# Performance work log

Measured on AMD Instinct MI355X. Metric: run time of the kernel, lower is better.

## Reference

```python
import jax, jax.numpy as jnp
import numpy as np

B, N, S = 256, 512, 32
D_ENT, D_KEY, D_IN, D_FUNC, D_TYPE, H = 256, 32, 1024, 256, 259, 32


def _init_linear(k, out_d, in_d):
    kw, kb = jax.random.split(k)
    bound = 1.0 / np.sqrt(in_d)
    W = jax.random.uniform(kw, (out_d, in_d), minval=-bound, maxval=bound, dtype=jnp.float32)
    b = jax.random.uniform(kb, (out_d,), minval=-bound, maxval=bound, dtype=jnp.float32)
    return W, b


def setup_inputs() -> dict:
    key = jax.random.key(0)
    ks = jax.random.split(key, 16)
    inp = {
        "embedding": jax.random.normal(ks[0], (B, D_IN), jnp.float32),
        "available_unit_type_mask": (jax.random.uniform(ks[1], (B, D_TYPE)) < 0.5).astype(jnp.float32),
        "available_units_mask": jnp.ones((B, N), jnp.float32),
        "entity_embedding": jax.random.normal(ks[2], (B, N, D_ENT), jnp.float32),
        "selected_units": jax.random.randint(ks[3], (B, S), 0, N, dtype=jnp.int32),
        "end_embedding": jax.random.uniform(ks[4], (1, D_KEY), minval=-1.0, maxval=1.0, dtype=jnp.float32) / np.sqrt(D_KEY),
    }
    inp["W_key"], inp["b_key"] = _init_linear(ks[5], D_KEY, D_ENT)
    inp["W_func"], inp["b_func"] = _init_linear(ks[6], D_FUNC, D_TYPE)
    inp["W_fc1"], inp["b_fc1"] = _init_linear(ks[7], D_FUNC, D_IN)
    inp["W_fc2"], inp["b_fc2"] = _init_linear(ks[8], D_KEY, D_FUNC)
    inp["W_embed"], inp["b_embed"] = _init_linear(ks[9], D_IN, D_KEY)
    inp["W_ih"], inp["b_ih"] = _init_linear(ks[10], 4 * H, D_KEY)
    inp["W_hh"], inp["b_hh"] = _init_linear(ks[11], 4 * H, H)
    return inp


def reference(embedding, available_unit_type_mask, available_units_mask, entity_embedding,
              selected_units, end_embedding, W_key, b_key, W_func, b_func, W_fc1, b_fc1,
              W_fc2, b_fc2, W_embed, b_embed, W_ih, b_ih, W_hh, b_hh):
    Bv, Nv, _ = entity_embedding.shape
    Sv = selected_units.shape[1]
    # keys for each entity + end-flag embedding appended -> [B, N+1, key_dim]
    key_t = jnp.einsum('bnd,kd->bnk', entity_embedding, W_key) + b_key
    end = jnp.broadcast_to(end_embedding[None, :, :], (Bv, 1, end_embedding.shape[1]))
    pad_key = jnp.concatenate([key_t, end], axis=1)
    # mask: entities + end flag; teacher-forced selected positions forced to 1
    mask0 = jnp.concatenate([available_units_mask, jnp.ones((Bv, 1), available_units_mask.dtype)], axis=1)
    mask0 = mask0.at[jnp.arange(Bv)[:, None], selected_units].set(1.0)
    func_embed = jax.nn.relu(available_unit_type_mask @ W_func.T + b_func)
    inv_n = 1.0 / jnp.float32(Nv)  # split_entity_num = end_flag_index = num_units
    bidx = jnp.arange(Bv)
    # per-step selected index (dummy 0 on the final end-flag step) and validity
    sel_seq = jnp.concatenate([selected_units.T, jnp.zeros((1, Bv), selected_units.dtype)], axis=0)
    valid_seq = jnp.concatenate([jnp.ones((Sv, Bv), jnp.float32), jnp.zeros((1, Bv), jnp.float32)], axis=0)

    def step(carry, xs):
        emb, h, c, mask = carry
        sel, valid = xs
        # query = fc2(relu(fc1(emb) + func_embed))
        x = jax.nn.relu(emb @ W_fc1.T + b_fc1 + func_embed) @ W_fc2.T + b_fc2
        # one LSTM step
        gates = x @ W_ih.T + b_ih + h @ W_hh.T + b_hh
        i_g, f_g, g_g, o_g = jnp.split(gates, 4, axis=1)
        c = jax.nn.sigmoid(f_g) * c + jax.nn.sigmoid(i_g) * jnp.tanh(g_g)
        h = jax.nn.sigmoid(o_g) * jnp.tanh(c)
        # masked dot-product over keys -> logits [B, N+1]
        q = jnp.einsum('bk,bnk->bn', h, pad_key) - (1.0 - mask) * 1e9
        # mark selected unit unavailable for subsequent steps
        mask = mask.at[bidx, sel].set(jnp.where(valid > 0, 0.0, mask[bidx, sel]))
        # one-hot gather of selected key, averaged, fed back into embedding
        emb_sel = pad_key[bidx, sel] * inv_n
        emb = emb + (emb_sel @ W_embed.T + b_embed) * valid[:, None]
        return (emb, h, c, mask), q

    h0 = jnp.zeros((Bv, W_hh.shape[1]), jnp.float32)
    c0 = jnp.zeros_like(h0)
    (emb, _, _, _), logits = jax.lax.scan(step, (embedding, h0, c0, mask0), (sel_seq, valid_seq))
    logits = jnp.transpose(logits, (1, 0, 2))  # [B, S+1, N+1]
    return logits, emb
```

## Files before the change

### kernel.cpp

```cpp
#include <hip/hip_runtime.h>
#include <math.h>

#define BB_ 256
#define NN_ 512
#define SS_ 32
#define NP1 513
#define SP1 33
#define D_IN 1024
#define D_TYPE 259
#define INV_N (1.0f/512.0f)

#define N_ACT 256
#define COMB_BASE 256
#define END_BID 258
#define KEY_BASE 259
#define N_KEY 2048
#define FRONT_GRID (KEY_BASE + N_KEY)

typedef short s16x4 __attribute__((ext_vector_type(4)));
typedef short s16x8 __attribute__((ext_vector_type(8)));
typedef float f32x4 __attribute__((ext_vector_type(4)));

#if defined(__has_builtin)
#if __has_builtin(__builtin_amdgcn_rcpf)
#define FRCP(x) __builtin_amdgcn_rcpf(x)
#else
#define FRCP(x) (1.0f / (x))
#endif
#else
#define FRCP(x) (1.0f / (x))
#endif

__device__ __forceinline__ float fsig(float x) { return FRCP(1.0f + __expf(-x)); }
__device__ __forceinline__ float ftanh(float x) { return fmaf(-2.0f, FRCP(1.0f + __expf(2.0f * x)), 1.0f); }
__device__ __forceinline__ short f2bf(float f) {
    unsigned u = __float_as_uint(f);
    unsigned r = (u + 0x7FFFu + ((u >> 16) & 1u)) >> 16;
    return (short)r;
}
__device__ __forceinline__ float bf2f(short s) {
    unsigned u = ((unsigned)(unsigned short)s) << 16;
    return __uint_as_float(u);
}

__global__ __launch_bounds__(256) void front_kernel(
    const float* __restrict__ ent, const float* __restrict__ Wk,
    const float* __restrict__ bk, const float* __restrict__ endv,
    const float* __restrict__ Wemb, const float* __restrict__ bemb,
    const float* __restrict__ Wfc1, const float* __restrict__ emb0,
    const float* __restrict__ bfc1, const float* __restrict__ atm,
    const float* __restrict__ Wf, const float* __restrict__ bf,
    short* __restrict__ pkbf, float* __restrict__ WcombT,
    float* __restrict__ cbv, float* __restrict__ act_pre)
{
    __shared__ __align__(128) char u_raw[33280];
    short* a_st   = (short*)u_raw;
    float* wemb_s = (float*)(u_raw + 18688);
    float* a_lds  = (float*)u_raw;
    float* w_lds  = (float*)(u_raw + 16640);

    const int tid = threadIdx.x;
    const int bid = blockIdx.x;
    const int lane = tid & 63, w = tid >> 6;
    const int nl = lane & 15, q = lane >> 4;

    if (bid >= KEY_BASE) {
        const size_t rowbase = (size_t)(bid - KEY_BASE) * 64;
        const int rl = w * 16 + nl;
        const float* arow = ent + ((rowbase + (size_t)rl) << 8) + q * 8;

        float4 aR[16];
#pragma unroll
        for (int kk = 0; kk < 8; kk++) {
            aR[kk * 2]     = *(const float4*)(arow + kk * 32);
            aR[kk * 2 + 1] = *(const float4*)(arow + kk * 32 + 4);
        }

        const float* brow0 = Wk + (size_t)nl * 256 + q * 8;
        const float* brow1 = Wk + (size_t)(16 + nl) * 256 + q * 8;

        f32x4 acc0 = (f32x4)0.0f, acc1 = (f32x4)0.0f;
#pragma unroll
        for (int kk = 0; kk < 8; kk++) {
            float4 b00 = *(const float4*)(brow0 + kk * 32);
            float4 b01 = *(const float4*)(brow0 + kk * 32 + 4);
            float4 b10 = *(const float4*)(brow1 + kk * 32);
            float4 b11 = *(const float4*)(brow1 + kk * 32 + 4);
            s16x8 af, bf0, bf1;
            float4 a0 = aR[kk * 2], a1 = aR[kk * 2 + 1];
            af[0] = f2bf(a0.x); af[1] = f2bf(a0.y); af[2] = f2bf(a0.z); af[3] = f2bf(a0.w);
            af[4] = f2bf(a1.x); af[5] = f2bf(a1.y); af[6] = f2bf(a1.z); af[7] = f2bf(a1.w);
            bf0[0] = f2bf(b00.x); bf0[1] = f2bf(b00.y); bf0[2] = f2bf(b00.z); bf0[3] = f2bf(b00.w);
            bf0[4] = f2bf(b01.x); bf0[5] = f2bf(b01.y); bf0[6] = f2bf(b01.z); bf0[7] = f2bf(b01.w);
            bf1[0] = f2bf(b10.x); bf1[1] = f2bf(b10.y); bf1[2] = f2bf(b10.z); bf1[3] = f2bf(b10.w);
            bf1[4] = f2bf(b11.x); bf1[5] = f2bf(b11.y); bf1[6] = f2bf(b11.z); bf1[7] = f2bf(b11.w);
            acc0 = __builtin_amdgcn_mfma_f32_16x16x32_bf16(af, bf0, acc0, 0, 0, 0);
            acc1 = __builtin_amdgcn_mfma_f32_16x16x32_bf16(af, bf1, acc1, 0, 0, 0);
        }

        float bkv0 = bk[nl], bkv1 = bk[16 + nl];
#pragma unroll
        for (int r = 0; r < 4; r++) {
            int rowg = (int)rowbase + w * 16 + q * 4 + r;
            int b = rowg >> 9, n = rowg & 511;
            pkbf[((size_t)b * NP1 + n) * 32 + nl]      = f2bf(acc0[r] + bkv0);
            pkbf[((size_t)b * NP1 + n) * 32 + 16 + nl] = f2bf(acc1[r] + bkv1);
        }
    } else if (bid < N_ACT) {
        const int idx = bid;
        const int jt = idx & 15, bt = idx >> 4;
        const int bb = tid >> 4, jj = tid & 15;

#pragma unroll 4
        for (int r = 0; r < 16; r++) {
            a_lds[r * 260 + tid] = atm[(size_t)(bt * 16 + r) * D_TYPE + tid];
            w_lds[r * 260 + tid] = Wf[(size_t)(jt * 16 + r) * D_TYPE + tid];
            if (tid < 3) {
                a_lds[r * 260 + 256 + tid] = atm[(size_t)(bt * 16 + r) * D_TYPE + 256 + tid];
                w_lds[r * 260 + 256 + tid] = Wf[(size_t)(jt * 16 + r) * D_TYPE + 256 + tid];
            }
        }
        __syncthreads();
        float accf;
        {
            float f0 = 0.0f, f1 = 0.0f, f2 = 0.0f, f3 = 0.0f;
            const float4* ap = (const float4*)&a_lds[bb * 260];
            const float4* wp = (const float4*)&w_lds[jj * 260];
#pragma unroll 8
            for (int i4 = 0; i4 < 64; i4++) {
                float4 a = ap[i4]; float4 wv = wp[i4];
                f0 = fmaf(a.x, wv.x, f0); f1 = fmaf(a.y, wv.y, f1);
                f2 = fmaf(a.z, wv.z, f2); f3 = fmaf(a.w, wv.w, f3);
            }
            accf = (f0 + f1) + (f2 + f3);
            for (int i = 256; i < 259; i++) accf = fmaf(a_lds[bb * 260 + i], w_lds[jj * 260 + i], accf);
        }
        float c0 = 0.0f, c1 = 0.0f, c2 = 0.0f, c3 = 0.0f;
        for (int c = 0; c < 4; c++) {
            __syncthreads();
#pragma unroll
            for (int p = 0; p < 4; p++) {
                int l4 = p * 256 + tid;
                int r = l4 >> 6, k4 = l4 & 63;
                *(float4*)&a_lds[r * 260 + k4 * 4] =
                    *(const float4*)(emb0 + (size_t)(bt * 16 + r) * D_IN + c * 256 + k4 * 4);
                *(float4*)&w_lds[r * 260 + k4 * 4] =
                    *(const float4*)(Wfc1 + (size_t)(jt * 16 + r) * D_IN + c * 256 + k4 * 4);
            }
            __syncthreads();
#pragma unroll 8
            for (int k4 = 0; k4 < 64; k4++) {
                float4 a = *(const float4*)&a_lds[bb * 260 + k4 * 4];
                float4 wv = *(const float4*)&w_lds[jj * 260 + k4 * 4];
                c0 = fmaf(a.x, wv.x, c0); c1 = fmaf(a.y, wv.y, c1);
                c2 = fmaf(a.z, wv.z, c2); c3 = fmaf(a.w, wv.w, c3);
            }
        }
        float acc = (c0 + c1) + (c2 + c3);
        const int b = bt * 16 + bb, j = jt * 16 + jj;
        act_pre[b * 256 + j] = acc + bfc1[j] + fmaxf(accf + bf[j], 0.0f);
    } else if (bid < END_BID) {
        const int m0 = bid - COMB_BASE;
        f32x4 acc[2][3];
#pragma unroll
        for (int mt = 0; mt < 2; mt++)
#pragma unroll
            for (int t = 0; t < 3; t++) acc[mt][t] = (f32x4)0.0f;

        for (int kc = 0; kc < 16; ++kc) {
            __syncthreads();
#pragma unroll
            for (int p = 0; p < 8; p++) {
                int flat = p * 256 + tid;
                int row = flat >> 4;
                int f4 = flat & 15;
                float4 v = *(const float4*)(Wfc1 + (size_t)(m0 * 128 + row) * D_IN + kc * 64 + f4 * 4);
                s16x4 sv;
                sv[0] = f2bf(v.x); sv[1] = f2bf(v.y); sv[2] = f2bf(v.z); sv[3] = f2bf(v.w);
                *(s16x4*)&a_st[row * 72 + f4 * 4] = sv;
            }
            {
                int r = tid >> 2, c0 = tid & 3;
#pragma unroll
                for (int cc = 0; cc < 9; cc++) {
                    int col = c0 + cc * 4;
                    if (col < 33) {
                        float v = (col < 32) ? Wemb[(size_t)(kc * 64 + r) * 32 + col]
                                             : bemb[kc * 64 + r];
                        wemb_s[r * 33 + col] = v;
                    }
                }
            }
            __syncthreads();
#pragma unroll
            for (int ks = 0; ks < 2; ks++) {
                s16x8 bv[3];
#pragma unroll
                for (int t = 0; t < 3; t++) {
                    int n = t * 16 + nl;
#pragma unroll
                    for (int jj = 0; jj < 8; jj++) {
                        float v = (n < 33) ? wemb_s[(ks * 32 + q * 8 + jj) * 33 + n] : 0.0f;
                        bv[t][jj] = f2bf(v);
                    }
                }
#pragma unroll
                for (int mt = 0; mt < 2; mt++) {
                    s16x8 af = *(const s16x8*)&a_st[(w * 32 + mt * 16 + nl) * 72 + ks * 32 + q * 8];
#pragma unroll
                    for (int t = 0; t < 3; t++)
                        acc[mt][t] = __builtin_amdgcn_mfma_f32_16x16x32_bf16(af, bv[t], acc[mt][t], 0, 0, 0);
                }
            }
        }
#pragma unroll
        for (int mt = 0; mt < 2; mt++)
#pragma unroll
            for (int t = 0; t < 3; t++)
#pragma unroll
                for (int r = 0; r < 4; r++) {
                    int j = m0 * 128 + w * 32 + mt * 16 + q * 4 + r;
                    int n = t * 16 + nl;
                    if (n < 32) WcombT[j * 32 + n] = acc[mt][t][r];
                    else if (n == 32) cbv[j] = acc[mt][t][r];
                }
    } else {
        const int k = tid & 31, b0 = tid >> 5;
        short evk = f2bf(endv[k]);
        for (int b = b0; b < BB_; b += 8)
            pkbf[((size_t)b * NP1 + 512) * 32 + k] = evk;
    }
}

__global__ __launch_bounds__(256, 1) void back_kernel(
    const short* __restrict__ pkbf, const float* __restrict__ act_pre0,
    const int* __restrict__ sel, const float* __restrict__ avail,
    const float* __restrict__ Wfc2, const float* __restrict__ bfc2,
    const float* __restrict__ Wih, const float* __restrict__ bih,
    const float* __restrict__ bhh, const float* __restrict__ Whh,
    const float* __restrict__ WcombT, const float* __restrict__ cbv,
    const float* __restrict__ emb0, const float* __restrict__ Wemb,
    const float* __restrict__ bemb,
    float* __restrict__ logits, float* __restrict__ emb_out)
{
    __shared__ float S[19204];
    __shared__ int sel_l[SS_];
    float* rap_l  = S;
    float* red_l  = S + 8580;
    float* x_l    = S + 17028;
    float* cumE_l = S + 18084;
    float* ssel_l = S + 19140;
    float* xg_l   = S;
    float* h_all  = S + 4224;
    float* m0_l   = S + 8580;
    int*   tf_l   = (int*)(S + 9093);

    const int tid = threadIdx.x;
    const int b = blockIdx.x;
    const int lane = tid & 63, w = tid >> 6;
    const int nl = lane & 15, q = lane >> 4;

    if (tid < SS_) sel_l[tid] = sel[b * SS_ + tid];

    {
        const int k = tid & 31, sq = tid >> 5;
        const int sq4 = sq * 4;
        int s0 = sel[b * SS_ + sq4 + 0];
        int s1 = sel[b * SS_ + sq4 + 1];
        int s2 = sel[b * SS_ + sq4 + 2];
        int s3 = sel[b * SS_ + sq4 + 3];
        float v0 = bf2f(pkbf[((size_t)b * NP1 + s0) * 32 + k]) * INV_N;
        float v1 = bf2f(pkbf[((size_t)b * NP1 + s1) * 32 + k]) * INV_N;
        float v2 = bf2f(pkbf[((size_t)b * NP1 + s2) * 32 + k]) * INV_N;
        float v3 = bf2f(pkbf[((size_t)b * NP1 + s3) * 32 + k]) * INV_N;
        float p0 = v0, p1 = p0 + v1, p2 = p1 + v2, p3 = p2 + v3;
        x_l[sq * 32 + k] = p3;
        __syncthreads();
        float off = 0.0f;
        for (int p = 0; p < 8; p++) if (p < sq) off += x_l[p * 32 + k];
        cumE_l[(sq4 + 1) * 32 + k] = off + p0;
        cumE_l[(sq4 + 2) * 32 + k] = off + p1;
        cumE_l[(sq4 + 3) * 32 + k] = off + p2;
        cumE_l[(sq4 + 4) * 32 + k] = off + p3;
        if (tid < 32) cumE_l[tid] = 0.0f;
        if (sq == 7) ssel_l[k] = off + p3;
    }
    __syncthreads();

    {
        float wcr[32];
#pragma unroll
        for (int k4 = 0; k4 < 8; k4++) {
            float4 v = *(const float4*)(WcombT + (size_t)tid * 32 + k4 * 4);
            wcr[k4*4] = v.x; wcr[k4*4+1] = v.y; wcr[k4*4+2] = v.z; wcr[k4*4+3] = v.w;
        }
        const float cbr = cbv[tid];
        const float ap0v = act_pre0[b * 256 + tid];
        for (int t = 0; t < SP1; ++t) {
            float ap = fmaf((float)t, cbr, ap0v);
            const float4* ce = (const float4*)&cumE_l[t * 32];
#pragma unroll
            for (int k4 = 0; k4 < 8; k4++) {
                float4 e = ce[k4];
                ap = fmaf(e.x, wcr[k4*4], ap);   ap = fmaf(e.y, wcr[k4*4+1], ap);
                ap = fmaf(e.z, wcr[k4*4+2], ap); ap = fmaf(e.w, wcr[k4*4+3], ap);
            }
            rap_l[t * 260 + tid] = fmaxf(ap, 0.0f);
        }
    }
    __syncthreads();

    {
        const int seg = tid >> 5, i = tid & 31;
        float wfc2r[32];
#pragma unroll
        for (int i4 = 0; i4 < 8; i4++) {
            float4 v = *(const float4*)(Wfc2 + (size_t)i * 256 + seg * 32 + i4 * 4);
            wfc2r[i4*4] = v.x; wfc2r[i4*4+1] = v.y; wfc2r[i4*4+2] = v.z; wfc2r[i4*4+3] = v.w;
        }
        for (int t = 0; t < SP1; ++t) {
            float part = 0.0f;
            const float4* rp = (const float4*)&rap_l[t * 260 + seg * 32];
#pragma unroll
            for (int i4 = 0; i4 < 8; i4++) {
                float4 rv = rp[i4];
                part = fmaf(rv.x, wfc2r[i4*4], part);   part = fmaf(rv.y, wfc2r[i4*4+1], part);
                part = fmaf(rv.z, wfc2r[i4*4+2], part); part = fmaf(rv.w, wfc2r[i4*4+3], part);
            }
            red_l[t * 256 + seg * 32 + i] = part;
        }
    }
    __syncthreads();

    for (int p = 0; p < 5; p++) {
        int idx = p * 256 + tid;
        if (idx < SP1 * 32) {
            int t = idx >> 5, i = idx & 31;
            float x = bfc2[i];
#pragma unroll
            for (int s = 0; s < 8; s++) x += red_l[t * 256 + s * 32 + i];
            x_l[t * 32 + i] = x;
        }
    }
    __syncthreads();

    {
        const int g = tid & 127, half = tid >> 7;
        float wihr[32];
#pragma unroll
        for (int k4 = 0; k4 < 8; k4++) {
            float4 v = *(const float4*)(Wih + (size_t)g * 32 + k4 * 4);
            wihr[k4*4] = v.x; wihr[k4*4+1] = v.y; wihr[k4*4+2] = v.z; wihr[k4*4+3] = v.w;
        }
        const float bihg = bih[g] + bhh[g];
        for (int t = half; t < SP1; t += 2) {
            float gg = bihg;
            const float4* xp = (const float4*)&x_l[t * 32];
#pragma unroll
            for (int k4 = 0; k4 < 8; k4++) {
                float4 xv = xp[k4];
                gg = fmaf(xv.x, wihr[k4*4], gg);   gg = fmaf(xv.y, wihr[k4*4+1], gg);
                gg = fmaf(xv.z, wihr[k4*4+2], gg); gg = fmaf(xv.w, wihr[k4*4+3], gg);
            }
            xg_l[t * 128 + g] = gg;
        }
    }
    __syncthreads();

    if (tid < 64) {
        float whh0[32], whh1[32];
#pragma unroll
        for (int k4 = 0; k4 < 8; k4++) {
            float4 v0 = *(const float4*)(Whh + (size_t)tid * 32 + k4 * 4);
            float4 v1 = *(const float4*)(Whh + (size_t)(tid + 64) * 32 + k4 * 4);
            whh0[k4*4] = v0.x; whh0[k4*4+1] = v0.y; whh0[k4*4+2] = v0.z; whh0[k4*4+3] = v0.w;
            whh1[k4*4] = v1.x; whh1[k4*4+1] = v1.y; whh1[k4*4+2] = v1.z; whh1[k4*4+3] = v1.w;
        }
        float c = 0.0f, h = 0.0f;
        for (int t = 0; t < SP1; ++t) {
            float g0 = xg_l[t * 128 + tid];
            float g1 = xg_l[t * 128 + 64 + tid];
            if (t > 0) {
#pragma unroll
                for (int k = 0; k < 32; k++) {
                    float hk = __shfl(h, k);
                    g0 = fmaf(hk, whh0[k], g0);
                    g1 = fmaf(hk, whh1[k], g1);
                }
            }
            float og0 = __shfl_xor(g0, 32);
            float og1 = __shfl_xor(g1, 32);
            float ig = fsig(g0);
            float fg = fsig(og0);
            float gv = ftanh(g1);
            float og = fsig(og1);
            float cn = fg * c + ig * gv;
            float hn = og * ftanh(cn);
            if (tid < 32) {
                c = cn; h = hn;
                h_all[t * 32 + tid] = hn;
            }
        }
    } else {
        for (int n = tid - 64; n < NP1; n += 192) {
            float m = (n < NN_) ? avail[(size_t)b * NN_ + n] : 1.0f;
            int tf = 1000;
#pragma unroll 8
            for (int s = 0; s < SS_; s++) {
                int sv = sel_l[s];
                if (sv == n) { m = 1.0f; if (s < tf) tf = s; }
            }
            m0_l[n] = m; tf_l[n] = tf;
        }
    }
    __syncthreads();

    {
        s16x8 afr[3];
#pragma unroll
        for (int mt = 0; mt < 3; mt++) {
            int row = mt * 16 + nl;
            s16x8 av;
#pragma unroll
            for (int jj = 0; jj < 8; jj++) {
                float v = (row < SP1) ? h_all[row * 32 + q * 8 + jj] : 0.0f;
                av[jj] = f2bf(v);
            }
            afr[mt] = av;
        }
        for (int tt = w; tt < 33; tt += 4) {
            int n = tt * 16 + nl;
            bool nv = n < NP1;
            s16x8 bv = nv ? *(const s16x8*)(pkbf + ((size_t)b * NP1 + n) * 32 + q * 8) : (s16x8)0;
            f32x4 acc[3];
#pragma unroll
            for (int mt = 0; mt < 3; mt++)
                acc[mt] = __builtin_amdgcn_mfma_f32_16x16x32_bf16(afr[mt], bv, (f32x4)0.0f, 0, 0, 0);
            float m0v = nv ? m0_l[n] : 0.0f;
            int tfv = nv ? tf_l[n] : 0;
#pragma unroll
            for (int mt = 0; mt < 3; mt++)
#pragma unroll
                for (int r = 0; r < 4; r++) {
                    int t = mt * 16 + q * 4 + r;
                    if (t < SP1 && nv) {
                        float mv = (t <= tfv) ? m0v : 0.0f;
                        logits[((size_t)b * SP1 + t) * NP1 + n] = acc[mt][r] - (1.0f - mv) * 1e9f;
                    }
                }
        }
    }

#pragma unroll
    for (int p = 0; p < 4; p++) {
        int i = p * 256 + tid;
        float acc = emb0[(size_t)b * D_IN + i] + 32.0f * bemb[i];
        const float* wr = Wemb + (size_t)i * 32;
#pragma unroll
        for (int k4 = 0; k4 < 8; k4++) {
            float4 wv = *(const float4*)(wr + k4 * 4);
            acc = fmaf(ssel_l[k4*4+0], wv.x, acc);
            acc = fmaf(ssel_l[k4*4+1], wv.y, acc);
            acc = fmaf(ssel_l[k4*4+2], wv.z, acc);
            acc = fmaf(ssel_l[k4*4+3], wv.w, acc);
        }
        emb_out[(size_t)b * D_IN + i] = acc;
    }
}

extern "C" void kernel_launch(void* const* d_in, const int* in_sizes, int n_in,
                              void* d_out, int out_size, void* d_ws, size_t ws_size,
                              hipStream_t stream)
{
    (void)in_sizes; (void)n_in; (void)out_size; (void)ws_size;
    const float* embedding = (const float*)d_in[0];
    const float* atm       = (const float*)d_in[1];
    const float* avail     = (const float*)d_in[2];
    const float* ent       = (const float*)d_in[3];
    const int*   sel       = (const int*)  d_in[4];
    const float* endv      = (const float*)d_in[5];
    const float* Wk   = (const float*)d_in[6];
    const float* bk   = (const float*)d_in[7];
    const float* Wf   = (const float*)d_in[8];
    const float* bf   = (const float*)d_in[9];
    const float* Wfc1 = (const float*)d_in[10];
    const float* bfc1 = (const float*)d_in[11];
    const float* Wfc2 = (const float*)d_in[12];
    const float* bfc2 = (const float*)d_in[13];
    const float* Wemb = (const float*)d_in[14];
    const float* bemb = (const float*)d_in[15];
    const float* Wih  = (const float*)d_in[16];
    const float* bih  = (const float*)d_in[17];
    const float* Whh  = (const float*)d_in[18];
    const float* bhh  = (const float*)d_in[19];

    float* ws = (float*)d_ws;
    float* act_pre = ws;
    float* WcombT  = act_pre + BB_ * 256;
    float* cbv     = WcombT + 256 * 32;
    short* pkbf    = (short*)(cbv + 256);

    float* logits  = (float*)d_out;
    float* emb_out = logits + (size_t)BB_ * SP1 * NP1;

    front_kernel<<<FRONT_GRID, 256, 0, stream>>>(ent, Wk, bk, endv, Wemb, bemb,
                                                 Wfc1, embedding, bfc1, atm, Wf, bf,
                                                 pkbf, WcombT, cbv, act_pre);
    back_kernel<<<BB_, 256, 0, stream>>>(pkbf, act_pre, sel, avail,
                                         Wfc2, bfc2, Wih, bih, bhh, Whh,
                                         WcombT, cbv, embedding, Wemb, bemb,
                                         logits, emb_out);
}
```

Baseline: 334.6 us.

## Split key projection into separate kernel with LDS-staged bf16 weights

Moves the entity-key projection out of the combined front kernel into its own kernel. Each block converts W_key to bf16 once into swizzled shared memory instead of having every thread reload and reconvert it from global memory. Entity-row loads are double-buffered to lower register pressure, and occupancy is raised through launch bounds. The cost is one extra kernel launch and a dependency boundary between the key and misc work, which previously ran in the same grid.

```diff
diff --git a/kernel.cpp b/kernel.cpp
--- a/kernel.cpp
+++ b/kernel.cpp
@@ -13,9 +13,8 @@
 #define N_ACT 256
 #define COMB_BASE 256
 #define END_BID 258
-#define KEY_BASE 259
+#define MISC_GRID 259
 #define N_KEY 2048
-#define FRONT_GRID (KEY_BASE + N_KEY)
 
 typedef short s16x4 __attribute__((ext_vector_type(4)));
 typedef short s16x8 __attribute__((ext_vector_type(8)));
@@ -43,9 +42,75 @@
     return __uint_as_float(u);
 }
 
-__global__ __launch_bounds__(256) void front_kernel(
+__global__ __launch_bounds__(256, 5) void keys_kernel(
     const float* __restrict__ ent, const float* __restrict__ Wk,
-    const float* __restrict__ bk, const float* __restrict__ endv,
+    const float* __restrict__ bk, short* __restrict__ pkbf)
+{
+    __shared__ short Bs[8192];
+
+    const int tid = threadIdx.x;
+    const int lane = tid & 63, w = tid >> 6;
+    const int nl = lane & 15, q = lane >> 4;
+
+#pragma unroll
+    for (int p = 0; p < 4; p++) {
+        int id = p * 256 + tid;
+        int n = id >> 5, cg = id & 31;
+        float4 v0 = *(const float4*)(Wk + (size_t)n * 256 + cg * 8);
+        float4 v1 = *(const float4*)(Wk + (size_t)n * 256 + cg * 8 + 4);
+        s16x8 sv;
+        sv[0] = f2bf(v0.x); sv[1] = f2bf(v0.y); sv[2] = f2bf(v0.z); sv[3] = f2bf(v0.w);
+        sv[4] = f2bf(v1.x); sv[5] = f2bf(v1.y); sv[6] = f2bf(v1.z); sv[7] = f2bf(v1.w);
+        int sw = (n & 7) << 1;
+        *(s16x8*)((char*)Bs + n * 512 + (((cg * 2) ^ sw) << 3)) = sv;
+    }
+    __syncthreads();
+
+    const int rl = w * 16 + nl;
+    const int swr = (nl & 7) << 1;
+#define BFRAG(t_, kk_) (*(const s16x8*)((const char*)Bs + \
+        (size_t)((t_) * 16 + nl) * 512 + ((((kk_) * 8 + q * 2) ^ swr) << 3)))
+
+    const size_t rowbase = (size_t)blockIdx.x * 64;
+    const float* arow = ent + ((rowbase + (size_t)rl) << 8) + q * 8;
+
+    float4 buf[4][2];
+#pragma unroll
+    for (int kk = 0; kk < 4; kk++) {
+        buf[kk][0] = *(const float4*)(arow + kk * 32);
+        buf[kk][1] = *(const float4*)(arow + kk * 32 + 4);
+    }
+
+    f32x4 acc0 = (f32x4)0.0f, acc1 = (f32x4)0.0f;
+#pragma unroll
+    for (int kk = 0; kk < 8; kk++) {
+        float4 a0 = buf[kk & 3][0], a1 = buf[kk & 3][1];
+        if (kk < 4) {
+            buf[kk & 3][0] = *(const float4*)(arow + (kk + 4) * 32);
+            buf[kk & 3][1] = *(const float4*)(arow + (kk + 4) * 32 + 4);
+        }
+        s16x8 af;
+        af[0] = f2bf(a0.x); af[1] = f2bf(a0.y); af[2] = f2bf(a0.z); af[3] = f2bf(a0.w);
+        af[4] = f2bf(a1.x); af[5] = f2bf(a1.y); af[6] = f2bf(a1.z); af[7] = f2bf(a1.w);
+        s16x8 b0 = BFRAG(0, kk);
+        s16x8 b1 = BFRAG(1, kk);
+        acc0 = __builtin_amdgcn_mfma_f32_16x16x32_bf16(af, b0, acc0, 0, 0, 0);
+        acc1 = __builtin_amdgcn_mfma_f32_16x16x32_bf16(af, b1, acc1, 0, 0, 0);
+    }
+#undef BFRAG
+
+    float bkv0 = bk[nl], bkv1 = bk[16 + nl];
+#pragma unroll
+    for (int r = 0; r < 4; r++) {
+        int rowg = (int)rowbase + w * 16 + q * 4 + r;
+        int b = rowg >> 9, n = rowg & 511;
+        pkbf[((size_t)b * NP1 + n) * 32 + nl]      = f2bf(acc0[r] + bkv0);
+        pkbf[((size_t)b * NP1 + n) * 32 + 16 + nl] = f2bf(acc1[r] + bkv1);
+    }
+}
+
+__global__ __launch_bounds__(256) void misc_kernel(
+    const float* __restrict__ endv,
     const float* __restrict__ Wemb, const float* __restrict__ bemb,
     const float* __restrict__ Wfc1, const float* __restrict__ emb0,
     const float* __restrict__ bfc1, const float* __restrict__ atm,
@@ -64,49 +129,7 @@
     const int lane = tid & 63, w = tid >> 6;
     const int nl = lane & 15, q = lane >> 4;
 
-    if (bid >= KEY_BASE) {
-        const size_t rowbase = (size_t)(bid - KEY_BASE) * 64;
-        const int rl = w * 16 + nl;
-        const float* arow = ent + ((rowbase + (size_t)rl) << 8) + q * 8;
-
-        float4 aR[16];
-#pragma unroll
-        for (int kk = 0; kk < 8; kk++) {
-            aR[kk * 2]     = *(const float4*)(arow + kk * 32);
-            aR[kk * 2 + 1] = *(const float4*)(arow + kk * 32 + 4);
-        }
-
-        const float* brow0 = Wk + (size_t)nl * 256 + q * 8;
-        const float* brow1 = Wk + (size_t)(16 + nl) * 256 + q * 8;
-
-        f32x4 acc0 = (f32x4)0.0f, acc1 = (f32x4)0.0f;
-#pragma unroll
-        for (int kk = 0; kk < 8; kk++) {
-            float4 b00 = *(const float4*)(brow0 + kk * 32);
-            float4 b01 = *(const float4*)(brow0 + kk * 32 + 4);
-            float4 b10 = *(const float4*)(brow1 + kk * 32);
-            float4 b11 = *(const float4*)(brow1 + kk * 32 + 4);
-            s16x8 af, bf0, bf1;
-            float4 a0 = aR[kk * 2], a1 = aR[kk * 2 + 1];
-            af[0] = f2bf(a0.x); af[1] = f2bf(a0.y); af[2] = f2bf(a0.z); af[3] = f2bf(a0.w);
-            af[4] = f2bf(a1.x); af[5] = f2bf(a1.y); af[6] = f2bf(a1.z); af[7] = f2bf(a1.w);
-            bf0[0] = f2bf(b00.x); bf0[1] = f2bf(b00.y); bf0[2] = f2bf(b00.z); bf0[3] = f2bf(b00.w);
-            bf0[4] = f2bf(b01.x); bf0[5] = f2bf(b01.y); bf0[6] = f2bf(b01.z); bf0[7] = f2bf(b01.w);
-            bf1[0] = f2bf(b10.x); bf1[1] = f2bf(b10.y); bf1[2] = f2bf(b10.z); bf1[3] = f2bf(b10.w);
-            bf1[4] = f2bf(b11.x); bf1[5] = f2bf(b11.y); bf1[6] = f2bf(b11.z); bf1[7] = f2bf(b11.w);
-            acc0 = __builtin_amdgcn_mfma_f32_16x16x32_bf16(af, bf0, acc0, 0, 0, 0);
-            acc1 = __builtin_amdgcn_mfma_f32_16x16x32_bf16(af, bf1, acc1, 0, 0, 0);
-        }
-
-        float bkv0 = bk[nl], bkv1 = bk[16 + nl];
-#pragma unroll
-        for (int r = 0; r < 4; r++) {
-            int rowg = (int)rowbase + w * 16 + q * 4 + r;
-            int b = rowg >> 9, n = rowg & 511;
-            pkbf[((size_t)b * NP1 + n) * 32 + nl]      = f2bf(acc0[r] + bkv0);
-            pkbf[((size_t)b * NP1 + n) * 32 + 16 + nl] = f2bf(acc1[r] + bkv1);
-        }
-    } else if (bid < N_ACT) {
+    if (bid < N_ACT) {
         const int idx = bid;
         const int jt = idx & 15, bt = idx >> 4;
         const int bb = tid >> 4, jj = tid & 15;
@@ -503,9 +526,10 @@
     float* logits  = (float*)d_out;
     float* emb_out = logits + (size_t)BB_ * SP1 * NP1;
 
-    front_kernel<<<FRONT_GRID, 256, 0, stream>>>(ent, Wk, bk, endv, Wemb, bemb,
-                                                 Wfc1, embedding, bfc1, atm, Wf, bf,
-                                                 pkbf, WcombT, cbv, act_pre);
+    keys_kernel<<<N_KEY, 256, 0, stream>>>(ent, Wk, bk, pkbf);
+    misc_kernel<<<MISC_GRID, 256, 0, stream>>>(endv, Wemb, bemb,
+                                               Wfc1, embedding, bfc1, atm, Wf, bf,
+                                               pkbf, WcombT, cbv, act_pre);
     back_kernel<<<BB_, 256, 0, stream>>>(pkbf, act_pre, sel, avail,
                                          Wfc2, bfc2, Wih, bih, bhh, Whh,
                                          WcombT, cbv, embedding, Wemb, bemb,
```

Measured after the change: 353.3 us. 1.06x slower.

## Split Wcomb reduction across blocks, hoist Wk fragments, reorder front grid

Applied to the files above, without the earlier changes.

The Wfc1·Wemb combination was computed by two blocks looping over 16 K-chunks. It is now split-K over 32 blocks that each handle one chunk and accumulate into zero-initialised outputs with atomicAdd, which removes a long serial tail from the front kernel. Key-projection blocks now come first in the grid, convert their Wk fragments to bf16 once before loading activations, and the kernel requests 4 blocks per CU through launch bounds. In exchange it adds a memset launch, float atomics that make the summation order nondeterministic, and more register pressure from the hoisted fragments.

```diff
diff --git a/kernel.cpp b/kernel.cpp
--- a/kernel.cpp
+++ b/kernel.cpp
@@ -10,12 +10,11 @@
 #define D_TYPE 259
 #define INV_N (1.0f/512.0f)
 
-#define N_ACT 256
-#define COMB_BASE 256
-#define END_BID 258
-#define KEY_BASE 259
 #define N_KEY 2048
-#define FRONT_GRID (KEY_BASE + N_KEY)
+#define ACT_BASE 2048
+#define COMB_BASE 2304
+#define END_BID 2336
+#define FRONT_GRID 2337
 
 typedef short s16x4 __attribute__((ext_vector_type(4)));
 typedef short s16x8 __attribute__((ext_vector_type(8)));
@@ -43,7 +42,7 @@
     return __uint_as_float(u);
 }
 
-__global__ __launch_bounds__(256) void front_kernel(
+__global__ __launch_bounds__(256, 4) void front_kernel(
     const float* __restrict__ ent, const float* __restrict__ Wk,
     const float* __restrict__ bk, const float* __restrict__ endv,
     const float* __restrict__ Wemb, const float* __restrict__ bemb,
@@ -64,38 +63,41 @@
     const int lane = tid & 63, w = tid >> 6;
     const int nl = lane & 15, q = lane >> 4;
 
-    if (bid >= KEY_BASE) {
-        const size_t rowbase = (size_t)(bid - KEY_BASE) * 64;
+    if (bid < N_KEY) {
+        const size_t rowbase = (size_t)bid * 64;
         const int rl = w * 16 + nl;
+
+        s16x8 bfr[8][2];
+#pragma unroll
+        for (int s = 0; s < 8; s++)
+#pragma unroll
+            for (int t = 0; t < 2; t++) {
+                const float* src = Wk + (size_t)(t * 16 + nl) * 256 + s * 32 + q * 8;
+                float4 v0 = *(const float4*)(src);
+                float4 v1 = *(const float4*)(src + 4);
+                s16x8 bv;
+                bv[0] = f2bf(v0.x); bv[1] = f2bf(v0.y); bv[2] = f2bf(v0.z); bv[3] = f2bf(v0.w);
+                bv[4] = f2bf(v1.x); bv[5] = f2bf(v1.y); bv[6] = f2bf(v1.z); bv[7] = f2bf(v1.w);
+                bfr[s][t] = bv;
+            }
+
         const float* arow = ent + ((rowbase + (size_t)rl) << 8) + q * 8;
-
         float4 aR[16];
 #pragma unroll
         for (int kk = 0; kk < 8; kk++) {
-            aR[kk * 2]     = *(const float4*)(arow + kk * 32);
-            aR[kk * 2 + 1] = *(const float4*)(arow + kk * 32 + 4);
-        }
-
-        const float* brow0 = Wk + (size_t)nl * 256 + q * 8;
-        const float* brow1 = Wk + (size_t)(16 + nl) * 256 + q * 8;
+            aR[2 * kk]     = *(const float4*)(arow + kk * 32);
+            aR[2 * kk + 1] = *(const float4*)(arow + kk * 32 + 4);
+        }
 
         f32x4 acc0 = (f32x4)0.0f, acc1 = (f32x4)0.0f;
 #pragma unroll
         for (int kk = 0; kk < 8; kk++) {
-            float4 b00 = *(const float4*)(brow0 + kk * 32);
-            float4 b01 = *(const float4*)(brow0 + kk * 32 + 4);
-            float4 b10 = *(const float4*)(brow1 + kk * 32);
-            float4 b11 = *(const float4*)(brow1 + kk * 32 + 4);
-            s16x8 af, bf0, bf1;
-            float4 a0 = aR[kk * 2], a1 = aR[kk * 2 + 1];
+            float4 a0 = aR[2 * kk], a1 = aR[2 * kk + 1];
+            s16x8 af;
             af[0] = f2bf(a0.x); af[1] = f2bf(a0.y); af[2] = f2bf(a0.z); af[3] = f2bf(a0.w);
             af[4] = f2bf(a1.x); af[5] = f2bf(a1.y); af[6] = f2bf(a1.z); af[7] = f2bf(a1.w);
-            bf0[0] = f2bf(b00.x); bf0[1] = f2bf(b00.y); bf0[2] = f2bf(b00.z); bf0[3] = f2bf(b00.w);
-            bf0[4] = f2bf(b01.x); bf0[5] = f2bf(b01.y); bf0[6] = f2bf(b01.z); bf0[7] = f2bf(b01.w);
-            bf1[0] = f2bf(b10.x); bf1[1] = f2bf(b10.y); bf1[2] = f2bf(b10.z); bf1[3] = f2bf(b10.w);
-            bf1[4] = f2bf(b11.x); bf1[5] = f2bf(b11.y); bf1[6] = f2bf(b11.z); bf1[7] = f2bf(b11.w);
-            acc0 = __builtin_amdgcn_mfma_f32_16x16x32_bf16(af, bf0, acc0, 0, 0, 0);
-            acc1 = __builtin_amdgcn_mfma_f32_16x16x32_bf16(af, bf1, acc1, 0, 0, 0);
+            acc0 = __builtin_amdgcn_mfma_f32_16x16x32_bf16(af, bfr[kk][0], acc0, 0, 0, 0);
+            acc1 = __builtin_amdgcn_mfma_f32_16x16x32_bf16(af, bfr[kk][1], acc1, 0, 0, 0);
         }
 
         float bkv0 = bk[nl], bkv1 = bk[16 + nl];
@@ -106,8 +108,8 @@
             pkbf[((size_t)b * NP1 + n) * 32 + nl]      = f2bf(acc0[r] + bkv0);
             pkbf[((size_t)b * NP1 + n) * 32 + 16 + nl] = f2bf(acc1[r] + bkv1);
         }
-    } else if (bid < N_ACT) {
-        const int idx = bid;
+    } else if (bid < COMB_BASE) {
+        const int idx = bid - ACT_BASE;
         const int jt = idx & 15, bt = idx >> 4;
         const int bb = tid >> 4, jj = tid & 15;
 
@@ -160,57 +162,58 @@
         const int b = bt * 16 + bb, j = jt * 16 + jj;
         act_pre[b * 256 + j] = acc + bfc1[j] + fmaxf(accf + bf[j], 0.0f);
     } else if (bid < END_BID) {
-        const int m0 = bid - COMB_BASE;
+        const int cb = bid - COMB_BASE;
+        const int kc = cb >> 1;
+        const int m0 = cb & 1;
+
+#pragma unroll
+        for (int p = 0; p < 8; p++) {
+            int flat = p * 256 + tid;
+            int row = flat >> 4;
+            int f4 = flat & 15;
+            float4 v = *(const float4*)(Wfc1 + (size_t)(m0 * 128 + row) * D_IN + kc * 64 + f4 * 4);
+            s16x4 sv;
+            sv[0] = f2bf(v.x); sv[1] = f2bf(v.y); sv[2] = f2bf(v.z); sv[3] = f2bf(v.w);
+            *(s16x4*)&a_st[row * 72 + f4 * 4] = sv;
+        }
+        {
+            int r = tid >> 2, c0 = tid & 3;
+#pragma unroll
+            for (int cc = 0; cc < 9; cc++) {
+                int col = c0 + cc * 4;
+                if (col < 33) {
+                    float v = (col < 32) ? Wemb[(size_t)(kc * 64 + r) * 32 + col]
+                                         : bemb[kc * 64 + r];
+                    wemb_s[r * 33 + col] = v;
+                }
+            }
+        }
+        __syncthreads();
+
         f32x4 acc[2][3];
 #pragma unroll
         for (int mt = 0; mt < 2; mt++)
 #pragma unroll
             for (int t = 0; t < 3; t++) acc[mt][t] = (f32x4)0.0f;
 
-        for (int kc = 0; kc < 16; ++kc) {
-            __syncthreads();
-#pragma unroll
-            for (int p = 0; p < 8; p++) {
-                int flat = p * 256 + tid;
-                int row = flat >> 4;
-                int f4 = flat & 15;
-                float4 v = *(const float4*)(Wfc1 + (size_t)(m0 * 128 + row) * D_IN + kc * 64 + f4 * 4);
-                s16x4 sv;
-                sv[0] = f2bf(v.x); sv[1] = f2bf(v.y); sv[2] = f2bf(v.z); sv[3] = f2bf(v.w);
-                *(s16x4*)&a_st[row * 72 + f4 * 4] = sv;
-            }
-            {
-                int r = tid >> 2, c0 = tid & 3;
-#pragma unroll
-                for (int cc = 0; cc < 9; cc++) {
-                    int col = c0 + cc * 4;
-                    if (col < 33) {
-                        float v = (col < 32) ? Wemb[(size_t)(kc * 64 + r) * 32 + col]
-                                             : bemb[kc * 64 + r];
-                        wemb_s[r * 33 + col] = v;
-                    }
+#pragma unroll
+        for (int ks = 0; ks < 2; ks++) {
+            s16x8 bv[3];
+#pragma unroll
+            for (int t = 0; t < 3; t++) {
+                int n = t * 16 + nl;
+#pragma unroll
+                for (int jj = 0; jj < 8; jj++) {
+                    float v = (n < 33) ? wemb_s[(ks * 32 + q * 8 + jj) * 33 + n] : 0.0f;
+                    bv[t][jj] = f2bf(v);
                 }
             }
-            __syncthreads();
-#pragma unroll
-            for (int ks = 0; ks < 2; ks++) {
-                s16x8 bv[3];
-#pragma unroll
-                for (int t = 0; t < 3; t++) {
-                    int n = t * 16 + nl;
-#pragma unroll
-                    for (int jj = 0; jj < 8; jj++) {
-                        float v = (n < 33) ? wemb_s[(ks * 32 + q * 8 + jj) * 33 + n] : 0.0f;
-                        bv[t][jj] = f2bf(v);
-                    }
-                }
-#pragma unroll
-                for (int mt = 0; mt < 2; mt++) {
-                    s16x8 af = *(const s16x8*)&a_st[(w * 32 + mt * 16 + nl) * 72 + ks * 32 + q * 8];
-#pragma unroll
-                    for (int t = 0; t < 3; t++)
-                        acc[mt][t] = __builtin_amdgcn_mfma_f32_16x16x32_bf16(af, bv[t], acc[mt][t], 0, 0, 0);
-                }
+#pragma unroll
+            for (int mt = 0; mt < 2; mt++) {
+                s16x8 af = *(const s16x8*)&a_st[(w * 32 + mt * 16 + nl) * 72 + ks * 32 + q * 8];
+#pragma unroll
+                for (int t = 0; t < 3; t++)
+                    acc[mt][t] = __builtin_amdgcn_mfma_f32_16x16x32_bf16(af, bv[t], acc[mt][t], 0, 0, 0);
             }
         }
 #pragma unroll
@@ -221,8 +224,8 @@
                 for (int r = 0; r < 4; r++) {
                     int j = m0 * 128 + w * 32 + mt * 16 + q * 4 + r;
                     int n = t * 16 + nl;
-                    if (n < 32) WcombT[j * 32 + n] = acc[mt][t][r];
-                    else if (n == 32) cbv[j] = acc[mt][t][r];
+                    if (n < 32) atomicAdd(&WcombT[j * 32 + n], acc[mt][t][r]);
+                    else if (n == 32) atomicAdd(&cbv[j], acc[mt][t][r]);
                 }
     } else {
         const int k = tid & 31, b0 = tid >> 5;
@@ -503,6 +506,8 @@
     float* logits  = (float*)d_out;
     float* emb_out = logits + (size_t)BB_ * SP1 * NP1;
 
+    hipMemsetAsync(WcombT, 0, (size_t)(256 * 32 + 256) * sizeof(float), stream);
+
     front_kernel<<<FRONT_GRID, 256, 0, stream>>>(ent, Wk, bk, endv, Wemb, bemb,
                                                  Wfc1, embedding, bfc1, atm, Wf, bf,
                                                  pkbf, WcombT, cbv, act_pre);
```

Measured after the change: 314.3 us. 1.06x faster.
